# Kernel tuning notes

Hardware: AMD Instinct MI355X
Metric: run time of the kernel (lower is better)

The kernel has to match this reference:

```python
import jax, jax.numpy as jnp
import numpy as np

K = 24            # patch_size (window)
D = 4             # dilation
C = 256           # dim
H = 8             # num_heads
N = 500000        # number of octree tokens at this depth (nnum_t)
BATCH_SIZE = 8
BLOCK = K * D
NA = int(np.ceil(N / BLOCK)) * BLOCK   # nnum_a (padded length)
PAD = NA - N
SCALE = (C // H) ** -0.5
MASK_VAL = -1000.0


def setup_inputs() -> dict:
    key = jax.random.key(0)
    k1, k2, k3, k4 = jax.random.split(key, 4)
    data = jax.random.normal(k1, (N, C), jnp.float32)
    qkv_w = jax.random.normal(k2, (3 * C, C), jnp.float32) * 0.02
    qkv_b = jnp.zeros((3 * C,), jnp.float32)
    proj_w = jax.random.normal(k3, (C, C), jnp.float32) * 0.02
    proj_b = jnp.zeros((C,), jnp.float32)
    batch_idx = jnp.sort(jax.random.randint(k4, (N,), 0, BATCH_SIZE, dtype=jnp.int32))
    return {"data": data, "qkv_w": qkv_w, "qkv_b": qkv_b,
            "proj_w": proj_w, "proj_b": proj_b, "batch_idx": batch_idx}


def _dilate_mask(batch_idx):
    # patch_partition of batch ids: pad with fill_value = batch_size
    b = jnp.concatenate([batch_idx, jnp.full((PAD,), BATCH_SIZE, jnp.int32)], axis=0)
    # dilate reshuffle: (-1, K, D) -> transpose -> (-1, K) windows
    b = b.reshape(-1, K, D).transpose(0, 2, 1).reshape(-1, K)
    diff = b[:, :, None] - b[:, None, :]           # [nw, K, K]
    return jnp.where(diff != 0, MASK_VAL, 0.0).astype(jnp.float32)


def reference(data, qkv_w, qkv_b, proj_w, proj_b, batch_idx):
    mask = _dilate_mask(batch_idx)                              # [nw, K, K]
    # patch_partition of features: pad with zeros
    x = jnp.concatenate([data, jnp.zeros((PAD, C), data.dtype)], axis=0)
    # dilation reshuffle: (-1, K, D, C) -> (-1, D, K, C) -> windows [nw, K, C]
    x = x.reshape(-1, K, D, C).transpose(0, 2, 1, 3).reshape(-1, K, C)
    qkv = (x @ qkv_w.T + qkv_b).reshape(-1, K, 3, H, C // H).transpose(2, 0, 3, 1, 4)
    q, k, v = qkv[0] * SCALE, qkv[1], qkv[2]                    # [nw, H, K, hd]
    attn = jnp.einsum('nhqd,nhkd->nhqk', q, k) + mask[:, None]  # [nw, H, K, K]
    attn = jax.nn.softmax(attn, axis=-1)
    out = jnp.einsum('nhqk,nhkd->nhqd', attn, v)
    out = out.transpose(0, 2, 1, 3).reshape(-1, C)              # merge heads
    # reverse dilation reshuffle, drop padding (patch_reverse)
    out = out.reshape(-1, D, K, C).transpose(0, 2, 1, 3).reshape(-1, C)[:N]
    return out @ proj_w.T + proj_b
```

## Files before the change

kernel.cpp:

```cpp
#include <hip/hip_runtime.h>


#define N_TOK 500000
#define NA    500064
#define MP    500096
#define MT    3907
#define MT8   3912
#define CDIM  256
#define KWIN  24
#define NWIN  20836
#define HEADS 8
#define SCALE_F 0.17677669529663689f

typedef __attribute__((ext_vector_type(8))) short bf16x8;
typedef __attribute__((ext_vector_type(4))) float f32x4;

__device__ __forceinline__ unsigned short f2b(float f) {
    unsigned int u = __float_as_uint(f);
    u += 0x7fffu + ((u >> 16) & 1u);
    return (unsigned short)(u >> 16);
}

#define GLOAD_LDS16(gsrc, ldst) \
    __builtin_amdgcn_global_load_lds((const __attribute__((address_space(1))) void*)(gsrc), \
                                     (__attribute__((address_space(3))) void*)(ldst), 16, 0, 0)


__global__ __launch_bounds__(256) void cvt_w_kernel(const float* __restrict__ src,
                                                    unsigned short* __restrict__ dst, int n8) {
    int i = blockIdx.x * 256 + threadIdx.x;
    if (i >= n8) return;
    float4 a = ((const float4*)src)[i * 2];
    float4 b = ((const float4*)src)[i * 2 + 1];
    uint4 o;
    o.x = (unsigned)f2b(a.x) | ((unsigned)f2b(a.y) << 16);
    o.y = (unsigned)f2b(a.z) | ((unsigned)f2b(a.w) << 16);
    o.z = (unsigned)f2b(b.x) | ((unsigned)f2b(b.y) << 16);
    o.w = (unsigned)f2b(b.z) | ((unsigned)f2b(b.w) << 16);
    ((uint4*)dst)[i] = o;
}

__global__ __launch_bounds__(256) void zero_pad_kernel(unsigned short* __restrict__ dst) {
    int i = blockIdx.x * 256 + threadIdx.x;
    if (i < (MP - N_TOK) * CDIM / 8)
        *(uint4*)(dst + (size_t)N_TOK * CDIM + (size_t)i * 8) = make_uint4(0u, 0u, 0u, 0u);
}


__global__ __launch_bounds__(256, 3) void qkv_gemm_kernel(const float* __restrict__ A32,
                                                          const unsigned short* __restrict__ Bt,
                                                          const float* __restrict__ bias,
                                                          unsigned short* __restrict__ out) {
    __shared__ unsigned short ldsA[128 * 64];
    __shared__ unsigned short ldsB[2][128 * 64];
    const int l = blockIdx.x;
    const int s = l >> 3;
    const int mtile = (l & 7) + 8 * (s / 6);
    const int ntile = s - (s / 6) * 6;
    if (mtile >= MT) return;

    const int tid  = threadIdx.x;
    const int lane = tid & 63;
    const int wv   = tid >> 6;
    const int wr   = wv >> 1, wc = wv & 1;

    f32x4 acc[4][4];
    #pragma unroll
    for (int i = 0; i < 4; ++i)
        #pragma unroll
        for (int j = 0; j < 4; ++j)
            #pragma unroll
            for (int r = 0; r < 4; ++r) acc[i][j][r] = 0.f;

    const char*  bbase = (const char*)(Bt + (size_t)ntile * 128 * CDIM);
    const int lrow8 = lane >> 3;
    const int lcolb = (lane & 7) * 16;
    const int arow  = tid >> 4;
    const int acol  = (tid & 15) * 4;
    const int growb = mtile * 128;
    const bool full_tile = (growb + 128 <= N_TOK);
    const float* aptr = A32 + (size_t)growb * CDIM + acol;

#define LOAD_A(kt_, dst_)                                                            \
    do {                                                                             \
        if (full_tile) {                                                             \
            _Pragma("unroll")                                                        \
            for (int i_ = 0; i_ < 8; ++i_)                                           \
                dst_[i_] = *(const float4*)(aptr + (size_t)(i_ * 16 + arow) * CDIM + (kt_) * 64); \
        } else {                                                                     \
            _Pragma("unroll")                                                        \
            for (int i_ = 0; i_ < 8; ++i_) {                                         \
                int rg_ = growb + i_ * 16 + arow;                                    \
                int rc_ = rg_ < N_TOK ? rg_ : (N_TOK - 1);                           \
                dst_[i_] = *(const float4*)(A32 + (size_t)rc_ * CDIM + (kt_) * 64 + acol); \
            }                                                                        \
            _Pragma("unroll")                                                        \
            for (int i_ = 0; i_ < 8; ++i_)                                           \
                if (growb + i_ * 16 + arow >= N_TOK) dst_[i_] = make_float4(0.f, 0.f, 0.f, 0.f); \
        }                                                                            \
    } while (0)

#define WRITE_A(src_)                                                                \
    do {                                                                             \
        _Pragma("unroll")                                                            \
        for (int i_ = 0; i_ < 8; ++i_) {                                             \
            float4 a_ = src_[i_];                                                    \
            uint2 o_;                                                                \
            o_.x = (unsigned)f2b(a_.x) | ((unsigned)f2b(a_.y) << 16);                \
            o_.y = (unsigned)f2b(a_.z) | ((unsigned)f2b(a_.w) << 16);                \
            *(uint2*)&ldsA[(i_ * 16 + arow) * 64 + acol] = o_;                       \
        }                                                                            \
    } while (0)

#define ISSUE_B(kt_, buf_)                                                           \
    do {                                                                             \
        _Pragma("unroll")                                                            \
        for (int c_ = 0; c_ < 4; ++c_) {                                             \
            int chunk_ = wv * 4 + c_;                                                \
            int row_ = chunk_ * 8 + lrow8;                                           \
            GLOAD_LDS16(bbase + (size_t)row_ * 512 + (kt_) * 128 + lcolb, &ldsB[buf_][chunk_ * 512]); \
        }                                                                            \
    } while (0)

    {
        float4 a0[8];
        LOAD_A(0, a0);
        ISSUE_B(0, 0);
        WRITE_A(a0);
    }
    __syncthreads();

    #pragma unroll
    for (int kt = 0; kt < 4; ++kt) {
        float4 anext[8];
        if (kt < 3) {
            LOAD_A(kt + 1, anext);
            ISSUE_B(kt + 1, (kt + 1) & 1);
        }
        #pragma unroll
        for (int ks = 0; ks < 2; ++ks) {
            const int kb = ks * 32 + (lane >> 4) * 8;
            bf16x8 af[4], bfr[4];
            #pragma unroll
            for (int i = 0; i < 4; ++i) {
                af[i]  = *(const bf16x8*)&ldsA[(wr * 64 + i * 16 + (lane & 15)) * 64 + kb];
                bfr[i] = *(const bf16x8*)&ldsB[kt & 1][(wc * 64 + i * 16 + (lane & 15)) * 64 + kb];
            }
            #pragma unroll
            for (int i = 0; i < 4; ++i)
                #pragma unroll
                for (int j = 0; j < 4; ++j)
                    acc[i][j] = __builtin_amdgcn_mfma_f32_16x16x32_bf16(af[i], bfr[j], acc[i][j], 0, 0, 0);
        }
        __syncthreads();
        if (kt < 3) {
            WRITE_A(anext);
            __syncthreads();
        }
    }
#undef LOAD_A
#undef WRITE_A
#undef ISSUE_B

    #pragma unroll
    for (int i = 0; i < 4; ++i) {
        int row0 = mtile * 128 + wr * 64 + i * 16 + ((lane >> 4) << 2);
        #pragma unroll
        for (int j = 0; j < 4; ++j) {
            int col = ntile * 128 + wc * 64 + j * 16 + (lane & 15);
            float bv = bias[col];
            #pragma unroll
            for (int r = 0; r < 4; ++r)
                out[(size_t)(row0 + r) * 768 + col] = f2b(acc[i][j][r] + bv);
        }
    }
}


__global__ __launch_bounds__(256, 3) void proj_gemm_kernel(const unsigned short* __restrict__ A,
                                                           const unsigned short* __restrict__ Bt,
                                                           const float* __restrict__ bias,
                                                           float* __restrict__ out) {
    __shared__ unsigned short ldsA[128 * 64];
    __shared__ unsigned short ldsB[128 * 64];
    const int l = blockIdx.x;
    const int s = l >> 3;
    const int mtile = (l & 7) + 8 * (s >> 1);
    const int ntile = s & 1;
    if (mtile >= MT) return;

    const int tid  = threadIdx.x;
    const int lane = tid & 63;
    const int wv   = tid >> 6;
    const int wr   = wv >> 1, wc = wv & 1;

    f32x4 acc[4][4];
    #pragma unroll
    for (int i = 0; i < 4; ++i)
        #pragma unroll
        for (int j = 0; j < 4; ++j)
            #pragma unroll
            for (int r = 0; r < 4; ++r) acc[i][j][r] = 0.f;

    const char* abase = (const char*)(A  + (size_t)mtile * 128 * CDIM);
    const char* bbase = (const char*)(Bt + (size_t)ntile * 128 * CDIM);
    const int lrow8 = lane >> 3;
    const int lcolb = (lane & 7) * 16;

    for (int kt = 0; kt < 4; ++kt) {
        const int kb_byte = kt * 128;
        #pragma unroll
        for (int c = 0; c < 4; ++c) {
            int chunk = wv * 4 + c;
            int row = chunk * 8 + lrow8;
            GLOAD_LDS16(abase + (size_t)row * 512 + kb_byte + lcolb, &ldsA[chunk * 512]);
        }
        #pragma unroll
        for (int c = 0; c < 4; ++c) {
            int chunk = wv * 4 + c;
            int row = chunk * 8 + lrow8;
            GLOAD_LDS16(bbase + (size_t)row * 512 + kb_byte + lcolb, &ldsB[chunk * 512]);
        }
        __syncthreads();
        #pragma unroll
        for (int ks = 0; ks < 2; ++ks) {
            const int kb = ks * 32 + (lane >> 4) * 8;
            bf16x8 af[4], bfr[4];
            #pragma unroll
            for (int i = 0; i < 4; ++i) {
                af[i]  = *(const bf16x8*)&ldsA[(wr * 64 + i * 16 + (lane & 15)) * 64 + kb];
                bfr[i] = *(const bf16x8*)&ldsB[(wc * 64 + i * 16 + (lane & 15)) * 64 + kb];
            }
            #pragma unroll
            for (int i = 0; i < 4; ++i)
                #pragma unroll
                for (int j = 0; j < 4; ++j)
                    acc[i][j] = __builtin_amdgcn_mfma_f32_16x16x32_bf16(af[i], bfr[j], acc[i][j], 0, 0, 0);
        }
        __syncthreads();
    }

    #pragma unroll
    for (int i = 0; i < 4; ++i) {
        int row0 = mtile * 128 + wr * 64 + i * 16 + ((lane >> 4) << 2);
        #pragma unroll
        for (int j = 0; j < 4; ++j) {
            int col = ntile * 128 + wc * 64 + j * 16 + (lane & 15);
            float bv = bias[col];
            #pragma unroll
            for (int r = 0; r < 4; ++r) {
                int row = row0 + r;
                if (row < N_TOK) out[(size_t)row * CDIM + col] = acc[i][j][r] + bv;
            }
        }
    }
}


__global__ __launch_bounds__(256) void attn_kernel(const unsigned short* __restrict__ qkv,
                                                   const int* __restrict__ batch_idx,
                                                   unsigned short* __restrict__ attn_out) {
    __shared__ unsigned short sP[4][32 * 64];
    const int tid  = threadIdx.x;
    const int lane = tid & 63;
    const int ws_  = tid >> 6;
    const int wid  = blockIdx.x * 4 + ws_;
    const int w = wid >> 3, h = wid & 7;
    const int gw = w >> 2, dd = w & 3;
    const int lrow = lane & 15, lg = lane >> 4;
    const int pbase = gw * 96 + dd;

    bf16x8 Qf[2], Kf[2];
    #pragma unroll
    for (int t = 0; t < 2; ++t) {
        size_t p = (size_t)(pbase + (t * 16 + lrow) * 4);
        const unsigned short* bp = qkv + p * 768 + h * 32 + lg * 8;
        Qf[t] = *(const bf16x8*)bp;
        Kf[t] = *(const bf16x8*)(bp + 256);
    }

    unsigned short v0[8], v1[8];
    #pragma unroll
    for (int j2 = 0; j2 < 8; ++j2) {
        size_t p = (size_t)(pbase + (lg * 8 + j2) * 4);
        const unsigned short* vp = qkv + p * 768 + 512 + h * 32 + lrow;
        v0[j2] = vp[0];
        v1[j2] = vp[16];
    }

    int bq[2];
    #pragma unroll
    for (int j = 0; j < 2; ++j) {
        int r = j * 16 + lrow;
        int p = pbase + r * 4;
        bq[j] = (r < KWIN && p < N_TOK) ? batch_idx[p] : -1;
    }
    int bk[2][4];
    #pragma unroll
    for (int i = 0; i < 2; ++i)
        #pragma unroll
        for (int rr = 0; rr < 4; ++rr) {
            int r = i * 16 + lg * 4 + rr;
            int p = pbase + r * 4;
            bk[i][rr] = (r < KWIN && p < N_TOK) ? batch_idx[p] : -2;
        }

    f32x4 accS[2][2];
    #pragma unroll
    for (int i = 0; i < 2; ++i)
        #pragma unroll
        for (int j = 0; j < 2; ++j)
            #pragma unroll
            for (int r = 0; r < 4; ++r) accS[i][j][r] = 0.f;
    #pragma unroll
    for (int i = 0; i < 2; ++i)
        #pragma unroll
        for (int j = 0; j < 2; ++j)
            accS[i][j] = __builtin_amdgcn_mfma_f32_16x16x32_bf16(Kf[i], Qf[j], accS[i][j], 0, 0, 0);

    float sv[2][2][4];
    float mx[2] = { -3.0e38f, -3.0e38f };
    #pragma unroll
    for (int i = 0; i < 2; ++i)
        #pragma unroll
        for (int j = 0; j < 2; ++j)
            #pragma unroll
            for (int rr = 0; rr < 4; ++rr) {
                float val = (bk[i][rr] == bq[j]) ? accS[i][j][rr] * SCALE_F : -1.0e9f;
                sv[i][j][rr] = val;
                mx[j] = fmaxf(mx[j], val);
            }
    mx[0] = fmaxf(mx[0], __shfl_xor(mx[0], 16)); mx[0] = fmaxf(mx[0], __shfl_xor(mx[0], 32));
    mx[1] = fmaxf(mx[1], __shfl_xor(mx[1], 16)); mx[1] = fmaxf(mx[1], __shfl_xor(mx[1], 32));
    float sm[2] = { 0.f, 0.f };
    #pragma unroll
    for (int i = 0; i < 2; ++i)
        #pragma unroll
        for (int j = 0; j < 2; ++j)
            #pragma unroll
            for (int rr = 0; rr < 4; ++rr) {
                float e = __expf(sv[i][j][rr] - mx[j]);
                sv[i][j][rr] = e;
                sm[j] += e;
            }
    sm[0] += __shfl_xor(sm[0], 16); sm[0] += __shfl_xor(sm[0], 32);
    sm[1] += __shfl_xor(sm[1], 16); sm[1] += __shfl_xor(sm[1], 32);
    float inv[2] = { 1.f / sm[0], 1.f / sm[1] };

    char* pb = (char*)sP[ws_];
    const int swz = (lrow & 7) << 4;
    #pragma unroll
    for (int j = 0; j < 2; ++j) {
        int q = j * 16 + lrow;
        #pragma unroll
        for (int i = 0; i < 2; ++i) {
            unsigned lo = (unsigned)f2b(sv[i][j][0] * inv[j]) | ((unsigned)f2b(sv[i][j][1] * inv[j]) << 16);
            unsigned hi = (unsigned)f2b(sv[i][j][2] * inv[j]) | ((unsigned)f2b(sv[i][j][3] * inv[j]) << 16);
            *(uint2*)(pb + q * 128 + ((i * 32 + lg * 8) ^ swz)) = make_uint2(lo, hi);
        }
    }
    bf16x8 AP[2];
    #pragma unroll
    for (int jj = 0; jj < 2; ++jj)
        AP[jj] = *(const bf16x8*)(pb + (jj * 16 + lrow) * 128 + ((lg * 16) ^ swz));

    union { bf16x8 v; unsigned short s[8]; } B0, B1;
    #pragma unroll
    for (int j2 = 0; j2 < 8; ++j2) { B0.s[j2] = v0[j2]; B1.s[j2] = v1[j2]; }
    f32x4 accO[2][2];
    #pragma unroll
    for (int i = 0; i < 2; ++i)
        #pragma unroll
        for (int j = 0; j < 2; ++j)
            #pragma unroll
            for (int r = 0; r < 4; ++r) accO[i][j][r] = 0.f;
    #pragma unroll
    for (int jj = 0; jj < 2; ++jj) {
        accO[jj][0] = __builtin_amdgcn_mfma_f32_16x16x32_bf16(AP[jj], B0.v, accO[jj][0], 0, 0, 0);
        accO[jj][1] = __builtin_amdgcn_mfma_f32_16x16x32_bf16(AP[jj], B1.v, accO[jj][1], 0, 0, 0);
    }

    #pragma unroll
    for (int jj = 0; jj < 2; ++jj)
        #pragma unroll
        for (int rr = 0; rr < 4; ++rr) {
            int q = jj * 16 + lg * 4 + rr;
            int p = pbase + q * 4;
            if (q < KWIN && p < N_TOK) {
                unsigned short* op = attn_out + (size_t)p * CDIM + h * 32;
                op[lrow]      = f2b(accO[jj][0][rr]);
                op[16 + lrow] = f2b(accO[jj][1][rr]);
            }
        }
}


extern "C" void kernel_launch(void* const* d_in, const int* in_sizes, int n_in,
                              void* d_out, int out_size, void* d_ws, size_t ws_size,
                              hipStream_t stream) {
    const float* data    = (const float*)d_in[0];
    const float* qkv_w   = (const float*)d_in[1];
    const float* qkv_b   = (const float*)d_in[2];
    const float* proj_w  = (const float*)d_in[3];
    const float* proj_b  = (const float*)d_in[4];
    const int*   batch_i = (const int*)d_in[5];

    char* ws = (char*)d_ws;
    size_t off = 0;
    unsigned short* qkvB   = (unsigned short*)(ws + off); off += (size_t)MP * 768 * 2;
    unsigned short* attnB  = (unsigned short*)(ws + off); off += (size_t)MP * CDIM * 2;
    unsigned short* wqkvB  = (unsigned short*)(ws + off); off += (size_t)768 * 256 * 2;
    unsigned short* wprojB = (unsigned short*)(ws + off); off += (size_t)256 * 256 * 2;
    if (ws_size < off) return;

    cvt_w_kernel<<<(768 * 256 / 8 + 255) / 256, 256, 0, stream>>>(qkv_w, wqkvB, 768 * 256 / 8);
    cvt_w_kernel<<<(256 * 256 / 8 + 255) / 256, 256, 0, stream>>>(proj_w, wprojB, 256 * 256 / 8);
    zero_pad_kernel<<<12, 256, 0, stream>>>(attnB);

    qkv_gemm_kernel<<<MT8 * 6, 256, 0, stream>>>(data, wqkvB, qkv_b, qkvB);
    attn_kernel<<<NWIN * HEADS / 4, 256, 0, stream>>>(qkvB, batch_i, attnB);
    proj_gemm_kernel<<<MT8 * 2, 256, 0, stream>>>(attnB, wprojB, proj_b, (float*)d_out);
}
```

Before: 1.052 ms.

## Double-buffer LDS and XOR-swizzle tiles in QKV and projection GEMMs

Both GEMM kernels now keep two LDS buffers for A and B. The next K-tile's global-to-LDS loads are issued before the MFMA work on the current tile, and one barrier per iteration is removed. LDS rows are stored with an XOR swizzle on the 16-byte column chunk to avoid bank conflicts on the bf16x8 fragment reads. The launch-bounds occupancy hint drops from 3 to 2 blocks per CU because LDS use per block grows.

```diff
diff --git a/kernel.cpp b/kernel.cpp
--- a/kernel.cpp
+++ b/kernel.cpp
@@ -47,11 +47,11 @@
 }
 
 
-__global__ __launch_bounds__(256, 3) void qkv_gemm_kernel(const float* __restrict__ A32,
+__global__ __launch_bounds__(256, 2) void qkv_gemm_kernel(const float* __restrict__ A32,
                                                           const unsigned short* __restrict__ Bt,
                                                           const float* __restrict__ bias,
                                                           unsigned short* __restrict__ out) {
-    __shared__ unsigned short ldsA[128 * 64];
+    __shared__ unsigned short ldsA[2][128 * 64];
     __shared__ unsigned short ldsB[2][128 * 64];
     const int l = blockIdx.x;
     const int s = l >> 3;
@@ -74,19 +74,23 @@
 
     const char*  bbase = (const char*)(Bt + (size_t)ntile * 128 * CDIM);
     const int lrow8 = lane >> 3;
-    const int lcolb = (lane & 7) * 16;
+    const int lcolb_sw = (((lane & 7) ^ lrow8) << 4);
     const int arow  = tid >> 4;
     const int acol  = (tid & 15) * 4;
+    const int awz   = (arow & 7) << 4;
     const int growb = mtile * 128;
     const bool full_tile = (growb + 128 <= N_TOK);
-    const float* aptr = A32 + (size_t)growb * CDIM + acol;
+    const int lrow = lane & 15, lg = lane >> 4;
+    const int swzr = (lrow & 7) << 4;
 
 #define LOAD_A(kt_, dst_)                                                            \
     do {                                                                             \
         if (full_tile) {                                                             \
             _Pragma("unroll")                                                        \
-            for (int i_ = 0; i_ < 8; ++i_)                                           \
-                dst_[i_] = *(const float4*)(aptr + (size_t)(i_ * 16 + arow) * CDIM + (kt_) * 64); \
+            for (int i_ = 0; i_ < 8; ++i_) {                                         \
+                int rg_ = growb + i_ * 16 + arow;                                    \
+                dst_[i_] = *(const float4*)(A32 + (size_t)rg_ * CDIM + (kt_) * 64 + acol); \
+            }                                                                        \
         } else {                                                                     \
             _Pragma("unroll")                                                        \
             for (int i_ = 0; i_ < 8; ++i_) {                                         \
@@ -100,15 +104,16 @@
         }                                                                            \
     } while (0)
 
-#define WRITE_A(src_)                                                                \
+#define WRITE_A(src_, buf_)                                                          \
     do {                                                                             \
+        char* ab_ = (char*)ldsA[buf_];                                               \
         _Pragma("unroll")                                                            \
         for (int i_ = 0; i_ < 8; ++i_) {                                             \
             float4 a_ = src_[i_];                                                    \
             uint2 o_;                                                                \
             o_.x = (unsigned)f2b(a_.x) | ((unsigned)f2b(a_.y) << 16);                \
             o_.y = (unsigned)f2b(a_.z) | ((unsigned)f2b(a_.w) << 16);                \
-            *(uint2*)&ldsA[(i_ * 16 + arow) * 64 + acol] = o_;                       \
+            *(uint2*)(ab_ + (i_ * 16 + arow) * 128 + (((tid & 15) * 8) ^ awz)) = o_; \
         }                                                                            \
     } while (0)
 
@@ -118,7 +123,7 @@
         for (int c_ = 0; c_ < 4; ++c_) {                                             \
             int chunk_ = wv * 4 + c_;                                                \
             int row_ = chunk_ * 8 + lrow8;                                           \
-            GLOAD_LDS16(bbase + (size_t)row_ * 512 + (kt_) * 128 + lcolb, &ldsB[buf_][chunk_ * 512]); \
+            GLOAD_LDS16(bbase + (size_t)row_ * 512 + (kt_) * 128 + lcolb_sw, &ldsB[buf_][chunk_ * 512]); \
         }                                                                            \
     } while (0)
 
@@ -126,25 +131,30 @@
         float4 a0[8];
         LOAD_A(0, a0);
         ISSUE_B(0, 0);
-        WRITE_A(a0);
+        WRITE_A(a0, 0);
     }
     __syncthreads();
 
+    int cur = 0;
     #pragma unroll
     for (int kt = 0; kt < 4; ++kt) {
         float4 anext[8];
         if (kt < 3) {
             LOAD_A(kt + 1, anext);
-            ISSUE_B(kt + 1, (kt + 1) & 1);
-        }
+            ISSUE_B(kt + 1, cur ^ 1);
+        }
+        const char* ab = (const char*)ldsA[cur];
+        const char* bb = (const char*)ldsB[cur];
         #pragma unroll
         for (int ks = 0; ks < 2; ++ks) {
-            const int kb = ks * 32 + (lane >> 4) * 8;
+            const int kbyte = ks * 64 + lg * 16;
             bf16x8 af[4], bfr[4];
             #pragma unroll
             for (int i = 0; i < 4; ++i) {
-                af[i]  = *(const bf16x8*)&ldsA[(wr * 64 + i * 16 + (lane & 15)) * 64 + kb];
-                bfr[i] = *(const bf16x8*)&ldsB[kt & 1][(wc * 64 + i * 16 + (lane & 15)) * 64 + kb];
+                int ra = wr * 64 + i * 16 + lrow;
+                int rb = wc * 64 + i * 16 + lrow;
+                af[i]  = *(const bf16x8*)(ab + ra * 128 + (kbyte ^ swzr));
+                bfr[i] = *(const bf16x8*)(bb + rb * 128 + (kbyte ^ swzr));
             }
             #pragma unroll
             for (int i = 0; i < 4; ++i)
@@ -152,10 +162,10 @@
                 for (int j = 0; j < 4; ++j)
                     acc[i][j] = __builtin_amdgcn_mfma_f32_16x16x32_bf16(af[i], bfr[j], acc[i][j], 0, 0, 0);
         }
-        __syncthreads();
         if (kt < 3) {
-            WRITE_A(anext);
+            WRITE_A(anext, cur ^ 1);
             __syncthreads();
+            cur ^= 1;
         }
     }
 #undef LOAD_A
@@ -164,10 +174,10 @@
 
     #pragma unroll
     for (int i = 0; i < 4; ++i) {
-        int row0 = mtile * 128 + wr * 64 + i * 16 + ((lane >> 4) << 2);
+        int row0 = mtile * 128 + wr * 64 + i * 16 + lg * 4;
         #pragma unroll
         for (int j = 0; j < 4; ++j) {
-            int col = ntile * 128 + wc * 64 + j * 16 + (lane & 15);
+            int col = ntile * 128 + wc * 64 + j * 16 + lrow;
             float bv = bias[col];
             #pragma unroll
             for (int r = 0; r < 4; ++r)
@@ -177,12 +187,12 @@
 }
 
 
-__global__ __launch_bounds__(256, 3) void proj_gemm_kernel(const unsigned short* __restrict__ A,
+__global__ __launch_bounds__(256, 2) void proj_gemm_kernel(const unsigned short* __restrict__ A,
                                                            const unsigned short* __restrict__ Bt,
                                                            const float* __restrict__ bias,
                                                            float* __restrict__ out) {
-    __shared__ unsigned short ldsA[128 * 64];
-    __shared__ unsigned short ldsB[128 * 64];
+    __shared__ unsigned short ldsA[2][128 * 64];
+    __shared__ unsigned short ldsB[2][128 * 64];
     const int l = blockIdx.x;
     const int s = l >> 3;
     const int mtile = (l & 7) + 8 * (s >> 1);
@@ -205,31 +215,40 @@
     const char* abase = (const char*)(A  + (size_t)mtile * 128 * CDIM);
     const char* bbase = (const char*)(Bt + (size_t)ntile * 128 * CDIM);
     const int lrow8 = lane >> 3;
-    const int lcolb = (lane & 7) * 16;
-
+    const int lcolb_sw = (((lane & 7) ^ lrow8) << 4);
+    const int lrow = lane & 15, lg = lane >> 4;
+    const int swzr = (lrow & 7) << 4;
+
+#define STAGE(kt_, buf_)                                                             \
+    do {                                                                             \
+        _Pragma("unroll")                                                            \
+        for (int c_ = 0; c_ < 4; ++c_) {                                             \
+            int chunk_ = wv * 4 + c_;                                                \
+            int row_ = chunk_ * 8 + lrow8;                                           \
+            GLOAD_LDS16(abase + (size_t)row_ * 512 + (kt_) * 128 + lcolb_sw, &ldsA[buf_][chunk_ * 512]); \
+            GLOAD_LDS16(bbase + (size_t)row_ * 512 + (kt_) * 128 + lcolb_sw, &ldsB[buf_][chunk_ * 512]); \
+        }                                                                            \
+    } while (0)
+
+    STAGE(0, 0);
+    __syncthreads();
+
+    int cur = 0;
+    #pragma unroll
     for (int kt = 0; kt < 4; ++kt) {
-        const int kb_byte = kt * 128;
-        #pragma unroll
-        for (int c = 0; c < 4; ++c) {
-            int chunk = wv * 4 + c;
-            int row = chunk * 8 + lrow8;
-            GLOAD_LDS16(abase + (size_t)row * 512 + kb_byte + lcolb, &ldsA[chunk * 512]);
-        }
-        #pragma unroll
-        for (int c = 0; c < 4; ++c) {
-            int chunk = wv * 4 + c;
-            int row = chunk * 8 + lrow8;
-            GLOAD_LDS16(bbase + (size_t)row * 512 + kb_byte + lcolb, &ldsB[chunk * 512]);
-        }
-        __syncthreads();
+        if (kt < 3) STAGE(kt + 1, cur ^ 1);
+        const char* ab = (const char*)ldsA[cur];
+        const char* bb = (const char*)ldsB[cur];
         #pragma unroll
         for (int ks = 0; ks < 2; ++ks) {
-            const int kb = ks * 32 + (lane >> 4) * 8;
+            const int kbyte = ks * 64 + lg * 16;
             bf16x8 af[4], bfr[4];
             #pragma unroll
             for (int i = 0; i < 4; ++i) {
-                af[i]  = *(const bf16x8*)&ldsA[(wr * 64 + i * 16 + (lane & 15)) * 64 + kb];
-                bfr[i] = *(const bf16x8*)&ldsB[(wc * 64 + i * 16 + (lane & 15)) * 64 + kb];
+                int ra = wr * 64 + i * 16 + lrow;
+                int rb = wc * 64 + i * 16 + lrow;
+                af[i]  = *(const bf16x8*)(ab + ra * 128 + (kbyte ^ swzr));
+                bfr[i] = *(const bf16x8*)(bb + rb * 128 + (kbyte ^ swzr));
             }
             #pragma unroll
             for (int i = 0; i < 4; ++i)
@@ -237,15 +256,19 @@
                 for (int j = 0; j < 4; ++j)
                     acc[i][j] = __builtin_amdgcn_mfma_f32_16x16x32_bf16(af[i], bfr[j], acc[i][j], 0, 0, 0);
         }
-        __syncthreads();
-    }
+        if (kt < 3) {
+            __syncthreads();
+            cur ^= 1;
+        }
+    }
+#undef STAGE
 
     #pragma unroll
     for (int i = 0; i < 4; ++i) {
-        int row0 = mtile * 128 + wr * 64 + i * 16 + ((lane >> 4) << 2);
+        int row0 = mtile * 128 + wr * 64 + i * 16 + lg * 4;
         #pragma unroll
         for (int j = 0; j < 4; ++j) {
-            int col = ntile * 128 + wc * 64 + j * 16 + (lane & 15);
+            int col = ntile * 128 + wc * 64 + j * 16 + lrow;
             float bv = bias[col];
             #pragma unroll
             for (int r = 0; r < 4; ++r) {
```

Result: no change. 1.068 ms (+1.5%).
